# Optimization experiments

Measured on AMD Instinct MI355X. Metric: run time of the kernel, lower is better.

The kernel has to match this reference:

```python
import jax, jax.numpy as jnp
import numpy as np

B = 64           # graph pairs
NPG = 48         # nodes per half-graph
N = B * 2 * NPG  # 6144 nodes
E = B * NPG * NPG  # 147456 directed mapping edges
DEG = 16
EG = N * DEG     # 98304 intra-graph edges
H = 128          # hidden dim (all layers)
HT = H // 2      # time embedding dim
L = 3            # num layers
G = 2 * B        # GraphNorm segments (bn_batch)


def _lin(k, i, o):
    return jax.random.normal(k, (i, o), jnp.float32) * (1.0 / np.sqrt(i))


def setup_inputs():
    key = jax.random.key(0)
    ks = list(jax.random.split(key, 64))
    rng = np.random.default_rng(0)
    inp = {}
    inp["graph_x"] = jax.random.normal(ks[0], (N, H), jnp.float32)
    inp["t"] = jnp.asarray(rng.integers(0, 1000, size=(B,)), jnp.float32)
    inp["noise_mapping_attr"] = jax.random.uniform(ks[1], (E,), jnp.float32)
    # intra-graph edges: random degree-DEG within each half-graph
    halves = np.arange(2 * B)
    bases = (halves // 2) * (2 * NPG) + (halves % 2) * NPG
    base_rep = np.repeat(bases, NPG * DEG)
    gsrc = base_rep + rng.integers(0, NPG, EG)
    gdst = base_rep + rng.integers(0, NPG, EG)
    inp["graph_edge_index"] = jnp.asarray(np.stack([gsrc, gdst]), jnp.int32)
    # full bipartite mapping edges graph1 -> graph2 within each pair
    p = np.repeat(np.arange(B), NPG * NPG)
    i = np.tile(np.repeat(np.arange(NPG), NPG), B)
    j = np.tile(np.tile(np.arange(NPG), NPG), B)
    inp["edge_mapping_idx"] = jnp.asarray(np.stack([p * 2 * NPG + i, p * 2 * NPG + NPG + j]), jnp.int32)
    inp["batch"] = jnp.asarray(np.repeat(np.arange(B), 2 * NPG), jnp.int32)
    inp["x_indicator"] = jnp.asarray(np.tile(np.r_[np.zeros(NPG, np.int32), np.ones(NPG, np.int32)], B), jnp.int32)
    # -------- learned parameters --------
    kit = iter(ks[2:])
    inp["gin_eps"] = jnp.zeros((L,), jnp.float32)
    inp["gin_w1"] = jnp.stack([_lin(next(kit), H, H) for _ in range(L)])
    inp["gin_b1"] = jnp.zeros((L, H), jnp.float32)
    inp["gin_w2"] = jnp.stack([_lin(next(kit), H, H) for _ in range(L)])
    inp["gin_b2"] = jnp.zeros((L, H), jnp.float32)
    inp["gn_w"] = jnp.ones((L, H), jnp.float32)
    inp["gn_b"] = jnp.zeros((L, H), jnp.float32)
    inp["gn_ms"] = jnp.ones((L, H), jnp.float32)
    for nm in ["ag_U", "ag_V", "ag_A", "ag_B", "ag_C"]:
        inp[nm] = jnp.stack([_lin(next(kit), H, H) for _ in range(L)])
        inp[nm + "b"] = jnp.zeros((L, H), jnp.float32)
    inp["ag_T"] = jnp.stack([_lin(next(kit), HT, H) for _ in range(L)])
    inp["ag_Tb"] = jnp.zeros((L, H), jnp.float32)
    inp["tw1"] = _lin(next(kit), H, HT); inp["tb1"] = jnp.zeros((HT,), jnp.float32)
    inp["tw2"] = _lin(next(kit), HT, HT); inp["tb2"] = jnp.zeros((HT,), jnp.float32)
    inp["ew"] = _lin(next(kit), H, H); inp["eb"] = jnp.zeros((H,), jnp.float32)
    inp["mw1"] = _lin(next(kit), H, 2 * H); inp["mb1"] = jnp.zeros((2 * H,), jnp.float32)
    inp["mw2"] = _lin(next(kit), 2 * H, H); inp["mb2"] = jnp.zeros((H,), jnp.float32)
    inp["mw3"] = _lin(next(kit), H, 1); inp["mb3"] = jnp.zeros((1,), jnp.float32)
    return inp


def _forward(graph_x, t, noise_mapping_attr, gin_eps, gin_w1, gin_b1, gin_w2, gin_b2,
             gn_w, gn_b, gn_ms, ag_U, ag_Ub, ag_V, ag_Vb, ag_A, ag_Ab, ag_B, ag_Bb,
             ag_C, ag_Cb, ag_T, ag_Tb, tw1, tb1, tw2, tb2, ew, eb,
             mw1, mb1, mw2, mb2, mw3, mb3,
             graph_edge_index, edge_mapping_idx, batch, x_indicator):
    seg = jax.ops.segment_sum
    # to_undirected on mapping edges: concat with flipped copy (graph1->graph2 only, so no dups)
    und = jnp.concatenate([edge_mapping_idx, edge_mapping_idx[::-1]], axis=1)   # [2, 2E]
    attr = jnp.concatenate([noise_mapping_attr, noise_mapping_attr])            # [2E]
    esrc, edst = und[0], und[1]
    gsrc, gdst = graph_edge_index[0], graph_edge_index[1]
    # diffusion timestep embedding -> time MLP (hidden -> H/2 -> H/2)
    half = H // 2
    freqs = jnp.exp(-jnp.log(10000.0) * jnp.arange(half, dtype=jnp.float32) / half)
    ang = t[:, None] * freqs
    temb = jnp.concatenate([jnp.cos(ang), jnp.sin(ang)], axis=-1)               # [B, H]
    temb = jnp.maximum(temb @ tw1 + tb1, 0.0) @ tw2 + tb2                       # [B, HT]
    # ScalarEmbeddingSine(normalize=False) on edge attrs, then edge_embed linear
    idx = jnp.arange(H)
    dim_t = 10000.0 ** (2.0 * (idx // 2).astype(jnp.float32) / H)
    pos = attr[:, None] / dim_t
    pe = jnp.stack([jnp.sin(pos[:, 0::2]), jnp.cos(pos[:, 1::2])], axis=2).reshape(-1, H)
    e = pe @ ew + eb                                                            # [2E, H]
    bn_batch = batch * 2 + x_indicator                                          # per half-graph segment ids
    e_batch = batch[esrc]                                                       # graph id per mapping edge
    h = graph_x
    for l in range(L):
        # GINConv (train_eps): nn((1+eps)*x + sum_{j->i} x_j)
        z = (1.0 + gin_eps[l]) * h + seg(h[gsrc], gdst, num_segments=N)
        z = jnp.maximum(z @ gin_w1[l] + gin_b1[l], 0.0) @ gin_w2[l] + gin_b2[l]
        # GraphNorm per half-graph, then ReLU
        cnt = seg(jnp.ones((N, 1), z.dtype), bn_batch, num_segments=G)
        mean = seg(z, bn_batch, num_segments=G) / cnt
        zc = z - mean[bn_batch] * gn_ms[l]
        var = seg(zc * zc, bn_batch, num_segments=G) / cnt
        h = jnp.maximum(gn_w[l] * zc / jnp.sqrt(var[bn_batch] + 1e-5) + gn_b[l], 0.0)
        # AGNN: anisotropic gated message passing over mapping edges, time-conditioned
        t_edge = temb[e_batch] @ ag_T[l] + ag_Tb[l]                              # [2E, H]
        e_new = (e @ ag_A[l] + ag_Ab[l]
                 + (h @ ag_B[l] + ag_Bb[l])[esrc]
                 + (h @ ag_C[l] + ag_Cb[l])[edst]
                 + t_edge)
        gate = jax.nn.sigmoid(e_new)
        magg = seg(gate * (h @ ag_V[l] + ag_Vb[l])[esrc], edst, num_segments=N)
        h = h + jnp.maximum(h @ ag_U[l] + ag_Ub[l] + magg, 0.0)
        e = e + jnp.maximum(e_new, 0.0)
    # readout MLP on edge features
    m = jnp.maximum(e @ mw1 + mb1, 0.0)
    m = jnp.maximum(m @ mw2 + mb2, 0.0)
    m = m @ mw3 + mb3                                                            # [2E, 1]
    half_e = m.shape[0] // 2
    # to_undirected coalesce(add) symmetrizes scores; keep edges with graph-1 source
    return m[:half_e] + m[half_e:]                                               # [E, 1]


def reference(graph_x, t, noise_mapping_attr, gin_eps, gin_w1, gin_b1, gin_w2, gin_b2,
              gn_w, gn_b, gn_ms, ag_U, ag_Ub, ag_V, ag_Vb, ag_A, ag_Ab, ag_B, ag_Bb,
              ag_C, ag_Cb, ag_T, ag_Tb, tw1, tb1, tw2, tb2, ew, eb,
              mw1, mb1, mw2, mb2, mw3, mb3,
              graph_edge_index, edge_mapping_idx, batch, x_indicator):
    return _forward(graph_x, t, noise_mapping_attr, gin_eps, gin_w1, gin_b1, gin_w2, gin_b2,
                    gn_w, gn_b, gn_ms, ag_U, ag_Ub, ag_V, ag_Vb, ag_A, ag_Ab, ag_B, ag_Bb,
                    ag_C, ag_Cb, ag_T, ag_Tb, tw1, tb1, tw2, tb2, ew, eb,
                    mw1, mb1, mw2, mb2, mw3, mb3,
                    graph_edge_index, edge_mapping_idx, batch, x_indicator)
```

## Files before the change

kernel.cpp:

```cpp
#include <hip/hip_runtime.h>
#include <cstdint>
#include <cstddef>

constexpr int kB   = 64;
constexpr int kNPG = 48;
constexpr int kN   = 6144;
constexpr int kE   = 147456;
constexpr int kE2  = 294912;
constexpr int kEG  = 98304;
constexpr int kH   = 128;
constexpr int kHT  = 64;
constexpr int kL   = 3;

using short8 = __attribute__((ext_vector_type(8))) short;
using f32x4  = __attribute__((ext_vector_type(4))) float;

__device__ __forceinline__ unsigned short f2bf(float x) {
    unsigned int u = __float_as_uint(x);
    u = (u + 0x7FFFu + ((u >> 16) & 1u)) >> 16;
    return (unsigned short)u;
}
__device__ __forceinline__ float bf2f(unsigned short v) {
    return __uint_as_float(((unsigned int)v) << 16);
}
__device__ __forceinline__ f32x4 mfma16(short8 a, short8 b, f32x4 c) {
    return __builtin_amdgcn_mfma_f32_16x16x32_bf16(a, b, c, 0, 0, 0);
}

__global__ void k_wprep(const float* __restrict__ W, unsigned short* __restrict__ Wf, int N) {
    int lane = threadIdx.x;
    int NT = N >> 4;
    int kt = blockIdx.x / NT, nt = blockIdx.x % NT;
    int k0 = kt * 32 + (lane >> 4) * 8;
    int col = nt * 16 + (lane & 15);
    unsigned short tmp[8];
    #pragma unroll
    for (int j = 0; j < 8; ++j) tmp[j] = f2bf(W[(size_t)(k0 + j) * N + col]);
    unsigned short* dst = Wf + (((size_t)blockIdx.x) * 64 + lane) * 8;
    *(uint4*)dst = *(const uint4*)tmp;
}

__global__ __launch_bounds__(256) void k_pegemm(const float* __restrict__ attr,
                                                const unsigned short* __restrict__ wf,
                                                const float* __restrict__ eb,
                                                uint32_t* __restrict__ e_packed) {
    int t = threadIdx.x, lane = t & 63, w = t >> 6;
    int rowbase = blockIdx.x * 64 + w * 16;
    int arow = rowbase + (lane & 15);
    float av = attr[arow < kE ? arow : arow - kE];
    f32x4 acc[8];
    #pragma unroll
    for (int nt = 0; nt < 8; ++nt) acc[nt] = (f32x4){0.f, 0.f, 0.f, 0.f};
    #pragma unroll
    for (int kt = 0; kt < 4; ++kt) {
        short8 ahi, alo;
        int k0 = kt * 32 + (lane >> 4) * 8;
        #pragma unroll
        for (int j = 0; j < 8; ++j) {
            int k = k0 + j;
            float freq = exp2f(-(float)(k >> 1) * 0.20762050593046264f);
            float ang = av * freq;
            float v = (k & 1) ? __cosf(ang) : __sinf(ang);
            unsigned short h = f2bf(v);
            unsigned short l2 = f2bf(v - bf2f(h));
            ahi[j] = (short)h; alo[j] = (short)l2;
        }
        #pragma unroll
        for (int nt = 0; nt < 8; ++nt) {
            short8 wb = *(const short8*)&wf[(((size_t)kt * 8 + nt) * 64 + lane) * 8];
            acc[nt] = mfma16(ahi, wb, acc[nt]);
            acc[nt] = mfma16(alo, wb, acc[nt]);
        }
    }
    #pragma unroll
    for (int nt = 0; nt < 8; ++nt) {
        int col = nt * 16 + (lane & 15);
        float bb = eb[col];
        #pragma unroll
        for (int reg = 0; reg < 4; ++reg) {
            int row = rowbase + (lane >> 4) * 4 + reg;
            float v = acc[nt][reg] + bb;
            unsigned short h = f2bf(v);
            unsigned short l2 = f2bf(v - bf2f(h));
            e_packed[(size_t)row * kH + col] = (uint32_t)h | ((uint32_t)l2 << 16);
        }
    }
}

__global__ __launch_bounds__(256) void k_egemm(uint32_t* __restrict__ e_packed,
                                               const unsigned short* __restrict__ wfA,
                                               const float* __restrict__ Ab,
                                               const float* __restrict__ tGl,
                                               const float* __restrict__ hB,
                                               const float* __restrict__ hC,
                                               unsigned short* __restrict__ gate) {
    __shared__ float X[48][128];
    __shared__ float Y[4][128];
    __shared__ float Z[128];
    int t = threadIdx.x, lane = t & 63, w = t >> 6;
    int row0 = blockIdx.x * 128;
    int half = row0 >= kE;
    int off = row0 - (half ? kE : 0);
    int p = off / 2304;
    int off2 = off - p * 2304;
    int a0 = off2 / 48, boff = off2 - a0 * 48;
    const float* Xsrc = half ? hB : hC;
    const float* Ysrc = half ? hC : hB;

    if (t < 128) Z[t] = tGl[p * kH + t] + Ab[t];
    for (int i = t; i < 48 * 32; i += 256) {
        int r = i >> 5, c = (i & 31) << 2;
        *(float4*)&X[r][c] = *(const float4*)&Xsrc[(size_t)(p * 96 + 48 + r) * kH + c];
    }
    for (int i = t; i < 4 * 32; i += 256) {
        int r = i >> 5, c = (i & 31) << 2;
        int a = a0 + r; if (a > 47) a = 47;
        *(float4*)&Y[r][c] = *(const float4*)&Ysrc[(size_t)(p * 96 + a) * kH + c];
    }
    __syncthreads();

    f32x4 acc[2][8];
    #pragma unroll
    for (int rt = 0; rt < 2; ++rt)
        #pragma unroll
        for (int nt = 0; nt < 8; ++nt) acc[rt][nt] = (f32x4){0.f, 0.f, 0.f, 0.f};

    #pragma unroll
    for (int kt = 0; kt < 4; ++kt) {
        short8 ahi[2], alo[2];
        #pragma unroll
        for (int rt = 0; rt < 2; ++rt) {
            int row = row0 + w * 32 + rt * 16 + (lane & 15);
            const uint32_t* ep = e_packed + (size_t)row * kH + kt * 32 + (lane >> 4) * 8;
            uint4 q0 = *(const uint4*)ep;
            uint4 q1 = *(const uint4*)(ep + 4);
            uint32_t qs[8] = {q0.x, q0.y, q0.z, q0.w, q1.x, q1.y, q1.z, q1.w};
            #pragma unroll
            for (int j = 0; j < 8; ++j) {
                ahi[rt][j] = (short)(qs[j] & 0xffff);
                alo[rt][j] = (short)(qs[j] >> 16);
            }
        }
        #pragma unroll
        for (int nt = 0; nt < 8; ++nt) {
            short8 wb = *(const short8*)&wfA[(((size_t)kt * 8 + nt) * 64 + lane) * 8];
            #pragma unroll
            for (int rt = 0; rt < 2; ++rt) {
                acc[rt][nt] = mfma16(ahi[rt], wb, acc[rt][nt]);
                acc[rt][nt] = mfma16(alo[rt], wb, acc[rt][nt]);
            }
        }
    }

    #pragma unroll
    for (int rt = 0; rt < 2; ++rt) {
        #pragma unroll
        for (int nt = 0; nt < 8; ++nt) {
            int col = nt * 16 + (lane & 15);
            float zc = Z[col];
            #pragma unroll
            for (int reg = 0; reg < 4; ++reg) {
                int rl = w * 32 + rt * 16 + (lane >> 4) * 4 + reg;
                int idx2 = boff + rl;
                int arel = (idx2 >= 144) ? 3 : (idx2 >= 96) ? 2 : (idx2 >= 48) ? 1 : 0;
                int b = idx2 - arel * 48;
                float v = acc[rt][nt][reg] + zc + Y[arel][col] + X[b][col];
                int grow = row0 + rl;
                float g = 1.f / (1.f + __expf(-v));
                gate[(size_t)grow * kH + col] = f2bf(g);
                uint32_t old = e_packed[(size_t)grow * kH + col];
                float oldv = bf2f((unsigned short)(old & 0xffff)) + bf2f((unsigned short)(old >> 16));
                float ne = oldv + fmaxf(v, 0.f);
                unsigned short h = f2bf(ne);
                unsigned short l2 = f2bf(ne - bf2f(h));
                e_packed[(size_t)grow * kH + col] = (uint32_t)h | ((uint32_t)l2 << 16);
            }
        }
    }
}

__global__ __launch_bounds__(256) void k_readout(const uint32_t* __restrict__ e_packed,
                                                 const unsigned short* __restrict__ wf1,
                                                 const float* __restrict__ mb1,
                                                 const unsigned short* __restrict__ wf2,
                                                 const float* __restrict__ mb2,
                                                 const float* __restrict__ mw3,
                                                 const float* __restrict__ mb3,
                                                 float* __restrict__ partial) {
    __shared__ char smem[64 * 528];
    uint32_t (*eS)[132] = (uint32_t(*)[132])smem;
    unsigned short (*m1S)[264] = (unsigned short(*)[264])smem;
    int t = threadIdx.x, lane = t & 63, w = t >> 6;
    int row0 = blockIdx.x * 64;

    for (int i = t; i < 64 * 32; i += 256) {
        int r = i >> 5, c = (i & 31) << 2;
        *(uint4*)&eS[r][c] = *(const uint4*)&e_packed[(size_t)(row0 + r) * kH + c];
    }
    __syncthreads();

    f32x4 acc1[4][4];
    #pragma unroll
    for (int rt = 0; rt < 4; ++rt)
        #pragma unroll
        for (int n = 0; n < 4; ++n) acc1[rt][n] = (f32x4){0.f, 0.f, 0.f, 0.f};
    #pragma unroll
    for (int kt = 0; kt < 4; ++kt) {
        short8 ahi[4], alo[4];
        #pragma unroll
        for (int rt = 0; rt < 4; ++rt) {
            int r = rt * 16 + (lane & 15);
            const uint32_t* ep = &eS[r][kt * 32 + (lane >> 4) * 8];
            #pragma unroll
            for (int j = 0; j < 8; ++j) {
                uint32_t q = ep[j];
                ahi[rt][j] = (short)(q & 0xffff);
                alo[rt][j] = (short)(q >> 16);
            }
        }
        #pragma unroll
        for (int n = 0; n < 4; ++n) {
            int nt = w * 4 + n;
            short8 wb = *(const short8*)&wf1[(((size_t)kt * 16 + nt) * 64 + lane) * 8];
            #pragma unroll
            for (int rt = 0; rt < 4; ++rt) {
                acc1[rt][n] = mfma16(ahi[rt], wb, acc1[rt][n]);
                acc1[rt][n] = mfma16(alo[rt], wb, acc1[rt][n]);
            }
        }
    }
    __syncthreads();
    #pragma unroll
    for (int rt = 0; rt < 4; ++rt) {
        #pragma unroll
        for (int n = 0; n < 4; ++n) {
            int col = (w * 4 + n) * 16 + (lane & 15);
            float bb = mb1[col];
            #pragma unroll
            for (int reg = 0; reg < 4; ++reg) {
                int r = rt * 16 + (lane >> 4) * 4 + reg;
                m1S[r][col] = f2bf(fmaxf(acc1[rt][n][reg] + bb, 0.f));
            }
        }
    }
    __syncthreads();

    f32x4 acc2[8];
    #pragma unroll
    for (int nt = 0; nt < 8; ++nt) acc2[nt] = (f32x4){0.f, 0.f, 0.f, 0.f};
    #pragma unroll
    for (int kt = 0; kt < 8; ++kt) {
        int r = w * 16 + (lane & 15);
        short8 a2 = *(const short8*)&m1S[r][kt * 32 + (lane >> 4) * 8];
        #pragma unroll
        for (int nt = 0; nt < 8; ++nt) {
            short8 wb = *(const short8*)&wf2[(((size_t)kt * 8 + nt) * 64 + lane) * 8];
            acc2[nt] = mfma16(a2, wb, acc2[nt]);
        }
    }
    float s[4] = {0.f, 0.f, 0.f, 0.f};
    #pragma unroll
    for (int nt = 0; nt < 8; ++nt) {
        int col = nt * 16 + (lane & 15);
        float w3 = mw3[col], bb = mb2[col];
        #pragma unroll
        for (int reg = 0; reg < 4; ++reg)
            s[reg] += fmaxf(acc2[nt][reg] + bb, 0.f) * w3;
    }
    #pragma unroll
    for (int mask = 1; mask <= 8; mask <<= 1)
        #pragma unroll
        for (int reg = 0; reg < 4; ++reg) s[reg] += __shfl_xor(s[reg], mask);
    if ((lane & 15) == 0) {
        float b3 = mb3[0];
        #pragma unroll
        for (int reg = 0; reg < 4; ++reg)
            partial[row0 + w * 16 + (lane >> 4) * 4 + reg] = s[reg] + b3;
    }
}

struct GemmPtrs { const float* W; const float* bias; float* C; };
struct GemmJobs { GemmPtrs j[4]; };

template<int MODE>
__global__ __launch_bounds__(256)
void k_gemm(const float* A, GemmJobs jobs, int M, int K, int Ncol)
{
    const GemmPtrs P = jobs.j[blockIdx.z];
    __shared__ float As[64][36];
    __shared__ float Ws[32][132];
    const int tid = threadIdx.x;
    const int tx = tid & 15, ty = tid >> 4;
    const int row0 = blockIdx.x * 64;
    const int colofs = blockIdx.y * 128;

    float acc[4][8];
    #pragma unroll
    for (int i = 0; i < 4; ++i)
        #pragma unroll
        for (int j = 0; j < 8; ++j) acc[i][j] = 0.f;

    for (int kk = 0; kk < K; kk += 32) {
        #pragma unroll
        for (int it = 0; it < 2; ++it) {
            int q = tid + it * 256;
            int r = q >> 3, kq = (q & 7) << 2;
            *(float4*)&As[r][kq] = *(const float4*)&A[(size_t)(row0 + r) * K + kk + kq];
        }
        #pragma unroll
        for (int it = 0; it < 4; ++it) {
            int q = tid + it * 256;
            int r = q >> 5, c = (q & 31) << 2;
            *(float4*)&Ws[r][c] = *(const float4*)&P.W[(size_t)(kk + r) * Ncol + colofs + c];
        }
        __syncthreads();
        #pragma unroll
        for (int k4 = 0; k4 < 8; ++k4) {
            float4 a[4];
            #pragma unroll
            for (int i = 0; i < 4; ++i)
                a[i] = *(const float4*)&As[ty * 4 + i][k4 * 4];
            float4 wv[4][2];
            #pragma unroll
            for (int k = 0; k < 4; ++k) {
                wv[k][0] = *(const float4*)&Ws[k4 * 4 + k][tx * 4];
                wv[k][1] = *(const float4*)&Ws[k4 * 4 + k][64 + tx * 4];
            }
            #pragma unroll
            for (int i = 0; i < 4; ++i) {
                #pragma unroll
                for (int k = 0; k < 4; ++k) {
                    float av = ((const float*)&a[i])[k];
                    acc[i][0] = fmaf(av, wv[k][0].x, acc[i][0]);
                    acc[i][1] = fmaf(av, wv[k][0].y, acc[i][1]);
                    acc[i][2] = fmaf(av, wv[k][0].z, acc[i][2]);
                    acc[i][3] = fmaf(av, wv[k][0].w, acc[i][3]);
                    acc[i][4] = fmaf(av, wv[k][1].x, acc[i][4]);
                    acc[i][5] = fmaf(av, wv[k][1].y, acc[i][5]);
                    acc[i][6] = fmaf(av, wv[k][1].z, acc[i][6]);
                    acc[i][7] = fmaf(av, wv[k][1].w, acc[i][7]);
                }
            }
        }
        __syncthreads();
    }

    #pragma unroll
    for (int i = 0; i < 4; ++i) {
        int row = row0 + ty * 4 + i;
        #pragma unroll
        for (int g = 0; g < 2; ++g) {
            int c = colofs + g * 64 + tx * 4;
            float4 vo;
            #pragma unroll
            for (int q = 0; q < 4; ++q) {
                float v = acc[i][g * 4 + q] + P.bias[c + q];
                if (MODE == 1) v = fmaxf(v, 0.f);
                ((float*)&vo)[q] = v;
            }
            *(float4*)&P.C[(size_t)row * Ncol + c] = vo;
        }
    }
}

__global__ void k_hist(const int* __restrict__ gdst, int* __restrict__ cnt) {
    int i = blockIdx.x * 256 + threadIdx.x;
    atomicAdd(&cnt[gdst[i]], 1);
}
__global__ void k_scan(const int* __restrict__ cnt, int* __restrict__ rs) {
    __shared__ int part[256];
    int t = threadIdx.x;
    const int per = kN / 256;
    int s = 0;
    for (int i = 0; i < per; ++i) s += cnt[t * per + i];
    part[t] = s;
    __syncthreads();
    if (t == 0) {
        int run = 0;
        for (int i = 0; i < 256; ++i) { int v = part[i]; part[i] = run; run += v; }
        rs[kN] = run;
    }
    __syncthreads();
    int run = part[t];
    for (int i = 0; i < per; ++i) { int idx = t * per + i; rs[idx] = run; run += cnt[idx]; }
}
__global__ void k_scatter(const int* __restrict__ gsrc, const int* __restrict__ gdst,
                          const int* __restrict__ rs, int* __restrict__ cur, int* __restrict__ csr) {
    int i = blockIdx.x * 256 + threadIdx.x;
    int d = gdst[i];
    int pos = atomicAdd(&cur[d], 1);
    csr[rs[d] + pos] = gsrc[i];
}
__global__ void k_gin(const float* __restrict__ h, const int* __restrict__ rs,
                      const int* __restrict__ csr, const float* __restrict__ gin_eps,
                      int l, float* __restrict__ z) {
    int n = blockIdx.x, c = threadIdx.x;
    int s0 = rs[n], s1 = rs[n + 1];
    float acc = 0.f;
    for (int k = s0; k < s1; ++k) acc += h[(size_t)csr[k] * kH + c];
    float eps = gin_eps[l];
    z[(size_t)n * kH + c] = (1.f + eps) * h[(size_t)n * kH + c] + acc;
}
__global__ void k_gnorm(const float* __restrict__ z, const float* __restrict__ gnw,
                        const float* __restrict__ gnb, const float* __restrict__ gnms,
                        float* __restrict__ h) {
    int g = blockIdx.x, c = threadIdx.x;
    size_t base = (size_t)g * 48 * kH + c;
    float sum = 0.f;
    for (int r = 0; r < 48; ++r) sum += z[base + (size_t)r * kH];
    float mean = sum * (1.f / 48.f);
    float mm = mean * gnms[c];
    float var = 0.f;
    for (int r = 0; r < 48; ++r) { float d = z[base + (size_t)r * kH] - mm; var = fmaf(d, d, var); }
    var *= (1.f / 48.f);
    float inv = rsqrtf(var + 1e-5f);
    float w = gnw[c], bb = gnb[c];
    for (int r = 0; r < 48; ++r) {
        float d = z[base + (size_t)r * kH] - mm;
        h[base + (size_t)r * kH] = fmaxf(fmaf(w * d, inv, bb), 0.f);
    }
}
__global__ void k_agg(const unsigned short* __restrict__ gate, const float* __restrict__ hV,
                      const float* __restrict__ hU, float* __restrict__ h) {
    int n = blockIdx.x, c = threadIdx.x;
    int p = n / 96, r = n - (n / 96) * 96;
    float acc = 0.f;
    if (r >= 48) {
        int b = r - 48;
        size_t ebase = (size_t)p * 2304 + b;
        for (int a = 0; a < 48; ++a) {
            size_t eidx = ebase + (size_t)a * 48;
            int src = p * 96 + a;
            acc = fmaf(bf2f(gate[eidx * kH + c]), hV[(size_t)src * kH + c], acc);
        }
    } else {
        int a = r;
        size_t ebase = (size_t)kE + (size_t)p * 2304 + (size_t)a * 48;
        for (int b = 0; b < 48; ++b) {
            int src = p * 96 + 48 + b;
            acc = fmaf(bf2f(gate[(ebase + b) * kH + c]), hV[(size_t)src * kH + c], acc);
        }
    }
    float v = hU[(size_t)n * kH + c] + acc;
    h[(size_t)n * kH + c] += fmaxf(v, 0.f);
}
__global__ void k_temb(const float* __restrict__ t, const float* __restrict__ tw1,
                       const float* __restrict__ tb1, const float* __restrict__ tw2,
                       const float* __restrict__ tb2, float* __restrict__ temb) {
    __shared__ float t0[128];
    __shared__ float h1[64];
    int b = blockIdx.x, j = threadIdx.x;
    float tv = t[b];
    float f = expf(-0.14391156831212787f * (float)j);
    float ang = tv * f;
    t0[j] = cosf(ang);
    t0[j + 64] = sinf(ang);
    __syncthreads();
    float s = tb1[j];
    for (int i = 0; i < 128; ++i) s = fmaf(t0[i], tw1[i * 64 + j], s);
    h1[j] = fmaxf(s, 0.f);
    __syncthreads();
    float s2 = tb2[j];
    for (int i = 0; i < 64; ++i) s2 = fmaf(h1[i], tw2[i * 64 + j], s2);
    temb[b * 64 + j] = s2;
}
__global__ void k_tg(const float* __restrict__ temb, const float* __restrict__ agT,
                     const float* __restrict__ agTb, float* __restrict__ tG) {
    __shared__ float tm[64];
    int bid = blockIdx.x;
    int l = bid >> 6, p = bid & 63, c = threadIdx.x;
    if (c < 64) tm[c] = temb[p * 64 + c];
    __syncthreads();
    const float* T = agT + (size_t)l * 64 * kH;
    float s = agTb[l * kH + c];
    for (int i = 0; i < 64; ++i) s = fmaf(tm[i], T[i * kH + c], s);
    tG[((size_t)l * 64 + p) * kH + c] = s;
}
__global__ void k_final(const float* __restrict__ partial, float* __restrict__ out) {
    int i = blockIdx.x * 256 + threadIdx.x;
    out[i] = partial[i] + partial[i + kE];
}

extern "C" void kernel_launch(void* const* d_in, const int* in_sizes, int n_in,
                              void* d_out, int out_size, void* d_ws, size_t ws_size,
                              hipStream_t stream)
{
    (void)in_sizes; (void)n_in; (void)out_size; (void)ws_size;
    const float* graph_x = (const float*)d_in[0];
    const float* t_in    = (const float*)d_in[1];
    const float* attr    = (const float*)d_in[2];
    const int*   gedge   = (const int*)d_in[3];
    const float* gin_eps = (const float*)d_in[7];
    const float* gin_w1  = (const float*)d_in[8];
    const float* gin_b1  = (const float*)d_in[9];
    const float* gin_w2  = (const float*)d_in[10];
    const float* gin_b2  = (const float*)d_in[11];
    const float* gn_w    = (const float*)d_in[12];
    const float* gn_b    = (const float*)d_in[13];
    const float* gn_ms   = (const float*)d_in[14];
    const float* ag_U    = (const float*)d_in[15];
    const float* ag_Ub   = (const float*)d_in[16];
    const float* ag_V    = (const float*)d_in[17];
    const float* ag_Vb   = (const float*)d_in[18];
    const float* ag_A    = (const float*)d_in[19];
    const float* ag_Ab   = (const float*)d_in[20];
    const float* ag_B    = (const float*)d_in[21];
    const float* ag_Bb   = (const float*)d_in[22];
    const float* ag_C    = (const float*)d_in[23];
    const float* ag_Cb   = (const float*)d_in[24];
    const float* ag_T    = (const float*)d_in[25];
    const float* ag_Tb   = (const float*)d_in[26];
    const float* tw1     = (const float*)d_in[27];
    const float* tb1     = (const float*)d_in[28];
    const float* tw2     = (const float*)d_in[29];
    const float* tb2     = (const float*)d_in[30];
    const float* ew      = (const float*)d_in[31];
    const float* eb      = (const float*)d_in[32];
    const float* mw1     = (const float*)d_in[33];
    const float* mb1     = (const float*)d_in[34];
    const float* mw2     = (const float*)d_in[35];
    const float* mb2     = (const float*)d_in[36];
    const float* mw3     = (const float*)d_in[37];
    const float* mb3     = (const float*)d_in[38];
    float* out = (float*)d_out;

    char* wsb = (char*)d_ws;
    size_t o = 0;
    auto carve = [&](size_t bytes) { char* p = wsb + o; o += (bytes + 255) & ~(size_t)255; return p; };
    uint32_t* e_packed    = (uint32_t*)carve((size_t)kE2 * kH * 4);
    unsigned short* gate  = (unsigned short*)carve((size_t)kE2 * kH * 2);
    float* h              = (float*)carve((size_t)kN * kH * 4);
    float* zb             = (float*)carve((size_t)kN * kH * 4);
    float* z1b            = (float*)carve((size_t)kN * kH * 4);
    float* hB             = (float*)carve((size_t)kN * kH * 4);
    float* hC             = (float*)carve((size_t)kN * kH * 4);
    float* hV             = (float*)carve((size_t)kN * kH * 4);
    float* hU             = (float*)carve((size_t)kN * kH * 4);
    float* temb           = (float*)carve((size_t)kB * kHT * 4);
    float* tG             = (float*)carve((size_t)kL * kB * kH * 4);
    float* partial        = (float*)carve((size_t)kE2 * 4);
    int* cnt              = (int*)carve((size_t)kN * 4);
    int* cur              = (int*)carve((size_t)kN * 4);
    int* rs               = (int*)carve((size_t)(kN + 1) * 4);
    int* csr              = (int*)carve((size_t)kEG * 4);
    unsigned short* wf_ew = (unsigned short*)carve((size_t)kH * kH * 2);
    unsigned short* wf_A  = (unsigned short*)carve((size_t)kL * kH * kH * 2);
    unsigned short* wf_m1 = (unsigned short*)carve((size_t)kH * 256 * 2);
    unsigned short* wf_m2 = (unsigned short*)carve((size_t)256 * kH * 2);

    const int* gsrc = gedge;
    const int* gdst = gedge + kEG;

    hipMemsetAsync(cnt, 0, (size_t)kN * 4, stream);
    hipMemsetAsync(cur, 0, (size_t)kN * 4, stream);
    hipMemcpyAsync(h, graph_x, (size_t)kN * kH * 4, hipMemcpyDeviceToDevice, stream);

    k_hist<<<kEG / 256, 256, 0, stream>>>(gdst, cnt);
    k_scan<<<1, 256, 0, stream>>>(cnt, rs);
    k_scatter<<<kEG / 256, 256, 0, stream>>>(gsrc, gdst, rs, cur, csr);
    k_temb<<<kB, 64, 0, stream>>>(t_in, tw1, tb1, tw2, tb2, temb);
    k_tg<<<kL * kB, kH, 0, stream>>>(temb, ag_T, ag_Tb, tG);

    k_wprep<<<4 * 8, 64, 0, stream>>>(ew, wf_ew, kH);
    for (int l = 0; l < kL; ++l)
        k_wprep<<<4 * 8, 64, 0, stream>>>(ag_A + (size_t)l * kH * kH, wf_A + (size_t)l * kH * kH, kH);
    k_wprep<<<4 * 16, 64, 0, stream>>>(mw1, wf_m1, 256);
    k_wprep<<<8 * 8, 64, 0, stream>>>(mw2, wf_m2, kH);

    k_pegemm<<<kE2 / 64, 256, 0, stream>>>(attr, wf_ew, eb, e_packed);

    for (int l = 0; l < kL; ++l) {
        k_gin<<<kN, kH, 0, stream>>>(h, rs, csr, gin_eps, l, zb);
        {
            GemmJobs jobs = {};
            jobs.j[0] = { gin_w1 + (size_t)l * kH * kH, gin_b1 + (size_t)l * kH, z1b };
            k_gemm<1><<<dim3(kN / 64, 1, 1), 256, 0, stream>>>(zb, jobs, kN, kH, kH);
        }
        {
            GemmJobs jobs = {};
            jobs.j[0] = { gin_w2 + (size_t)l * kH * kH, gin_b2 + (size_t)l * kH, zb };
            k_gemm<0><<<dim3(kN / 64, 1, 1), 256, 0, stream>>>(z1b, jobs, kN, kH, kH);
        }
        k_gnorm<<<128, kH, 0, stream>>>(zb, gn_w + (size_t)l * kH, gn_b + (size_t)l * kH,
                                        gn_ms + (size_t)l * kH, h);
        {
            GemmJobs jobs = {};
            jobs.j[0] = { ag_B + (size_t)l * kH * kH, ag_Bb + (size_t)l * kH, hB };
            jobs.j[1] = { ag_C + (size_t)l * kH * kH, ag_Cb + (size_t)l * kH, hC };
            jobs.j[2] = { ag_V + (size_t)l * kH * kH, ag_Vb + (size_t)l * kH, hV };
            jobs.j[3] = { ag_U + (size_t)l * kH * kH, ag_Ub + (size_t)l * kH, hU };
            k_gemm<0><<<dim3(kN / 64, 1, 4), 256, 0, stream>>>(h, jobs, kN, kH, kH);
        }
        k_egemm<<<kE2 / 128, 256, 0, stream>>>(e_packed, wf_A + (size_t)l * kH * kH,
                                               ag_Ab + (size_t)l * kH, tG + (size_t)l * kB * kH,
                                               hB, hC, gate);
        k_agg<<<kN, kH, 0, stream>>>(gate, hV, hU, h);
    }

    k_readout<<<kE2 / 64, 256, 0, stream>>>(e_packed, wf_m1, mb1, wf_m2, mb2, mw3, mb3, partial);
    k_final<<<kE / 256, 256, 0, stream>>>(partial, out);
}
```

Before: 941.0 us.

## Fuse per-graph node pipeline into one MFMA kernel and skip unused final aggregation

The per-layer node path (GIN neighbour sum, two GIN linear layers, GraphNorm, and the four B/C/V/U projections) is merged into a single kernel with one block per 48-node half-graph. Intermediates stay in shared memory, and the fp32 FMA GEMMs become split-bf16 MFMA GEMMs. All 22 square weight matrices are converted in one batched prep launch. In the last layer the gate store and the node aggregation are skipped, because only edge features feed the readout. The fused kernel launches only 128 blocks and each uses just three of its four waves for the MFMA stages, which trades parallelism for fewer launches and less global traffic.

```diff
diff --git a/kernel.cpp b/kernel.cpp
--- a/kernel.cpp
+++ b/kernel.cpp
@@ -23,8 +23,20 @@
 __device__ __forceinline__ float bf2f(unsigned short v) {
     return __uint_as_float(((unsigned int)v) << 16);
 }
+__device__ __forceinline__ uint32_t packsplit(float v) {
+    unsigned short h = f2bf(v);
+    unsigned short l = f2bf(v - bf2f(h));
+    return (uint32_t)h | ((uint32_t)l << 16);
+}
 __device__ __forceinline__ f32x4 mfma16(short8 a, short8 b, f32x4 c) {
     return __builtin_amdgcn_mfma_f32_16x16x32_bf16(a, b, c, 0, 0, 0);
+}
+__device__ __forceinline__ void loadfrag(const uint32_t* p, short8& hi, short8& lo) {
+    uint4 q0 = *(const uint4*)p;
+    uint4 q1 = *(const uint4*)(p + 4);
+    uint32_t qs[8] = {q0.x, q0.y, q0.z, q0.w, q1.x, q1.y, q1.z, q1.w};
+    #pragma unroll
+    for (int j = 0; j < 8; ++j) { hi[j] = (short)(qs[j] & 0xffff); lo[j] = (short)(qs[j] >> 16); }
 }
 
 __global__ void k_wprep(const float* __restrict__ W, unsigned short* __restrict__ Wf, int N) {
@@ -37,6 +49,21 @@
     #pragma unroll
     for (int j = 0; j < 8; ++j) tmp[j] = f2bf(W[(size_t)(k0 + j) * N + col]);
     unsigned short* dst = Wf + (((size_t)blockIdx.x) * 64 + lane) * 8;
+    *(uint4*)dst = *(const uint4*)tmp;
+}
+
+struct WSrcs { const float* p[22]; };
+__global__ void k_wprep_multi(WSrcs s, unsigned short* __restrict__ Wf) {
+    int lane = threadIdx.x;
+    int mat = blockIdx.x >> 5, tile = blockIdx.x & 31;
+    int kt = tile >> 3, nt = tile & 7;
+    const float* W = s.p[mat];
+    int k0 = kt * 32 + (lane >> 4) * 8;
+    int col = nt * 16 + (lane & 15);
+    unsigned short tmp[8];
+    #pragma unroll
+    for (int j = 0; j < 8; ++j) tmp[j] = f2bf(W[(size_t)(k0 + j) * kH + col]);
+    unsigned short* dst = Wf + (size_t)mat * 16384 + (((size_t)tile) * 64 + lane) * 8;
     *(uint4*)dst = *(const uint4*)tmp;
 }
 
@@ -79,14 +106,190 @@
         #pragma unroll
         for (int reg = 0; reg < 4; ++reg) {
             int row = rowbase + (lane >> 4) * 4 + reg;
-            float v = acc[nt][reg] + bb;
-            unsigned short h = f2bf(v);
-            unsigned short l2 = f2bf(v - bf2f(h));
-            e_packed[(size_t)row * kH + col] = (uint32_t)h | ((uint32_t)l2 << 16);
-        }
-    }
-}
-
+            e_packed[(size_t)row * kH + col] = packsplit(acc[nt][reg] + bb);
+        }
+    }
+}
+
+__global__ __launch_bounds__(256) void k_node(
+    float* __restrict__ h,
+    int l, const int* __restrict__ rs, const int* __restrict__ csr,
+    const float* __restrict__ gin_eps,
+    const unsigned short* __restrict__ wf_g1, const float* __restrict__ b1,
+    const unsigned short* __restrict__ wf_g2, const float* __restrict__ b2,
+    const float* __restrict__ gnw, const float* __restrict__ gnb, const float* __restrict__ gnms,
+    const unsigned short* __restrict__ wf_B, const float* __restrict__ Bb,
+    const unsigned short* __restrict__ wf_C, const float* __restrict__ Cb,
+    const unsigned short* __restrict__ wf_V, const float* __restrict__ Vb,
+    const unsigned short* __restrict__ wf_U, const float* __restrict__ Ub,
+    float* __restrict__ hB, float* __restrict__ hC, float* __restrict__ hV, float* __restrict__ hU)
+{
+    __shared__ char sA[48 * 132 * 4];
+    __shared__ char sB[48 * 132 * 4];
+    __shared__ float mmS[128], aS[128], red0[128], red1[128];
+    float    (*hS)[132]   = (float(*)[132])sA;
+    uint32_t (*m1pk)[132] = (uint32_t(*)[132])sA;
+    uint32_t (*hnpk)[132] = (uint32_t(*)[132])sA;
+    uint32_t (*zpk)[132]  = (uint32_t(*)[132])sB;
+    float    (*z2S)[132]  = (float(*)[132])sB;
+    int t = threadIdx.x, lane = t & 63, w = t >> 6;
+    int g = blockIdx.x, nbase = g * 48;
+
+    for (int i = t; i < 48 * 128; i += 256) {
+        int r = i >> 7, c = i & 127;
+        hS[r][c] = h[(size_t)(nbase + r) * kH + c];
+    }
+    __syncthreads();
+
+    {
+        float eps1 = 1.f + gin_eps[l];
+        int c = t & 127;
+        for (int rp = t >> 7; rp < 48; rp += 2) {
+            float acc = eps1 * hS[rp][c];
+            int s0 = rs[nbase + rp], s1 = rs[nbase + rp + 1];
+            for (int k = s0; k < s1; ++k) {
+                int s = csr[k] - nbase;
+                acc += hS[s][c];
+            }
+            zpk[rp][c] = packsplit(acc);
+        }
+    }
+    __syncthreads();
+
+    {
+        f32x4 acc1[8];
+        if (w < 3) {
+            #pragma unroll
+            for (int nt = 0; nt < 8; ++nt) acc1[nt] = (f32x4){0.f, 0.f, 0.f, 0.f};
+            #pragma unroll
+            for (int kt = 0; kt < 4; ++kt) {
+                short8 hi, lo;
+                loadfrag(&zpk[w * 16 + (lane & 15)][kt * 32 + (lane >> 4) * 8], hi, lo);
+                #pragma unroll
+                for (int nt = 0; nt < 8; ++nt) {
+                    short8 wb = *(const short8*)&wf_g1[(((size_t)kt * 8 + nt) * 64 + lane) * 8];
+                    acc1[nt] = mfma16(hi, wb, acc1[nt]);
+                    acc1[nt] = mfma16(lo, wb, acc1[nt]);
+                }
+            }
+        }
+        __syncthreads();
+        if (w < 3) {
+            #pragma unroll
+            for (int nt = 0; nt < 8; ++nt) {
+                int col = nt * 16 + (lane & 15);
+                float bb = b1[col];
+                #pragma unroll
+                for (int reg = 0; reg < 4; ++reg) {
+                    int row = w * 16 + (lane >> 4) * 4 + reg;
+                    m1pk[row][col] = packsplit(fmaxf(acc1[nt][reg] + bb, 0.f));
+                }
+            }
+        }
+    }
+    __syncthreads();
+
+    {
+        f32x4 acc2[8];
+        if (w < 3) {
+            #pragma unroll
+            for (int nt = 0; nt < 8; ++nt) acc2[nt] = (f32x4){0.f, 0.f, 0.f, 0.f};
+            #pragma unroll
+            for (int kt = 0; kt < 4; ++kt) {
+                short8 hi, lo;
+                loadfrag(&m1pk[w * 16 + (lane & 15)][kt * 32 + (lane >> 4) * 8], hi, lo);
+                #pragma unroll
+                for (int nt = 0; nt < 8; ++nt) {
+                    short8 wb = *(const short8*)&wf_g2[(((size_t)kt * 8 + nt) * 64 + lane) * 8];
+                    acc2[nt] = mfma16(hi, wb, acc2[nt]);
+                    acc2[nt] = mfma16(lo, wb, acc2[nt]);
+                }
+            }
+        }
+        __syncthreads();
+        if (w < 3) {
+            #pragma unroll
+            for (int nt = 0; nt < 8; ++nt) {
+                int col = nt * 16 + (lane & 15);
+                float bb = b2[col];
+                #pragma unroll
+                for (int reg = 0; reg < 4; ++reg) {
+                    int row = w * 16 + (lane >> 4) * 4 + reg;
+                    z2S[row][col] = acc2[nt][reg] + bb;
+                }
+            }
+        }
+    }
+    __syncthreads();
+
+    {
+        int c = t & 127, hh = t >> 7;
+        float s = 0.f;
+        for (int r = hh * 24; r < hh * 24 + 24; ++r) s += z2S[r][c];
+        if (hh == 0) red0[c] = s; else red1[c] = s;
+        __syncthreads();
+        if (t < 128) {
+            float mean = (red0[t] + red1[t]) * (1.f / 48.f);
+            mmS[t] = mean * gnms[t];
+        }
+        __syncthreads();
+        float mm = mmS[c];
+        float s2 = 0.f;
+        for (int r = hh * 24; r < hh * 24 + 24; ++r) { float d = z2S[r][c] - mm; s2 = fmaf(d, d, s2); }
+        if (hh == 0) red0[c] = s2; else red1[c] = s2;
+        __syncthreads();
+        if (t < 128) {
+            float var = (red0[t] + red1[t]) * (1.f / 48.f);
+            aS[t] = gnw[t] * rsqrtf(var + 1e-5f);
+        }
+    }
+    __syncthreads();
+
+    for (int i = t; i < 48 * 128; i += 256) {
+        int r = i >> 7, c = i & 127;
+        float hn = fmaxf(aS[c] * (z2S[r][c] - mmS[c]) + gnb[c], 0.f);
+        h[(size_t)(nbase + r) * kH + c] = hn;
+        hnpk[r][c] = packsplit(hn);
+    }
+    __syncthreads();
+
+    {
+        const unsigned short* wfs[4] = {wf_B, wf_C, wf_V, wf_U};
+        const float* bs[4] = {Bb, Cb, Vb, Ub};
+        float* outs[4] = {hB, hC, hV, hU};
+        #pragma unroll 4
+        for (int m = 0; m < 4; ++m) {
+            if (w < 3) {
+                f32x4 accp[8];
+                #pragma unroll
+                for (int nt = 0; nt < 8; ++nt) accp[nt] = (f32x4){0.f, 0.f, 0.f, 0.f};
+                #pragma unroll
+                for (int kt = 0; kt < 4; ++kt) {
+                    short8 hi, lo;
+                    loadfrag(&hnpk[w * 16 + (lane & 15)][kt * 32 + (lane >> 4) * 8], hi, lo);
+                    #pragma unroll
+                    for (int nt = 0; nt < 8; ++nt) {
+                        short8 wb = *(const short8*)&wfs[m][(((size_t)kt * 8 + nt) * 64 + lane) * 8];
+                        accp[nt] = mfma16(hi, wb, accp[nt]);
+                        accp[nt] = mfma16(lo, wb, accp[nt]);
+                    }
+                }
+                #pragma unroll
+                for (int nt = 0; nt < 8; ++nt) {
+                    int col = nt * 16 + (lane & 15);
+                    float bb = bs[m][col];
+                    #pragma unroll
+                    for (int reg = 0; reg < 4; ++reg) {
+                        int row = w * 16 + (lane >> 4) * 4 + reg;
+                        outs[m][(size_t)(nbase + row) * kH + col] = accp[nt][reg] + bb;
+                    }
+                }
+            }
+        }
+    }
+}
+
+template<bool GATE>
 __global__ __launch_bounds__(256) void k_egemm(uint32_t* __restrict__ e_packed,
                                                const unsigned short* __restrict__ wfA,
                                                const float* __restrict__ Ab,
@@ -127,27 +330,19 @@
 
     #pragma unroll
     for (int kt = 0; kt < 4; ++kt) {
-        short8 ahi[2], alo[2];
+        short8 hi[2], lo[2];
         #pragma unroll
         for (int rt = 0; rt < 2; ++rt) {
             int row = row0 + w * 32 + rt * 16 + (lane & 15);
-            const uint32_t* ep = e_packed + (size_t)row * kH + kt * 32 + (lane >> 4) * 8;
-            uint4 q0 = *(const uint4*)ep;
-            uint4 q1 = *(const uint4*)(ep + 4);
-            uint32_t qs[8] = {q0.x, q0.y, q0.z, q0.w, q1.x, q1.y, q1.z, q1.w};
-            #pragma unroll
-            for (int j = 0; j < 8; ++j) {
-                ahi[rt][j] = (short)(qs[j] & 0xffff);
-                alo[rt][j] = (short)(qs[j] >> 16);
-            }
+            loadfrag(e_packed + (size_t)row * kH + kt * 32 + (lane >> 4) * 8, hi[rt], lo[rt]);
         }
         #pragma unroll
         for (int nt = 0; nt < 8; ++nt) {
             short8 wb = *(const short8*)&wfA[(((size_t)kt * 8 + nt) * 64 + lane) * 8];
             #pragma unroll
             for (int rt = 0; rt < 2; ++rt) {
-                acc[rt][nt] = mfma16(ahi[rt], wb, acc[rt][nt]);
-                acc[rt][nt] = mfma16(alo[rt], wb, acc[rt][nt]);
+                acc[rt][nt] = mfma16(hi[rt], wb, acc[rt][nt]);
+                acc[rt][nt] = mfma16(lo[rt], wb, acc[rt][nt]);
             }
         }
     }
@@ -166,17 +361,42 @@
                 int b = idx2 - arel * 48;
                 float v = acc[rt][nt][reg] + zc + Y[arel][col] + X[b][col];
                 int grow = row0 + rl;
-                float g = 1.f / (1.f + __expf(-v));
-                gate[(size_t)grow * kH + col] = f2bf(g);
+                if (GATE) {
+                    float g = 1.f / (1.f + __expf(-v));
+                    gate[(size_t)grow * kH + col] = f2bf(g);
+                }
                 uint32_t old = e_packed[(size_t)grow * kH + col];
-                float oldv = bf2f((unsigned short)(old & 0xffff)) + bf2f((unsigned short)(old >> 16));
-                float ne = oldv + fmaxf(v, 0.f);
-                unsigned short h = f2bf(ne);
-                unsigned short l2 = f2bf(ne - bf2f(h));
-                e_packed[(size_t)grow * kH + col] = (uint32_t)h | ((uint32_t)l2 << 16);
-            }
-        }
-    }
+                float ne = bf2f((unsigned short)(old & 0xffff)) + bf2f((unsigned short)(old >> 16))
+                           + fmaxf(v, 0.f);
+                e_packed[(size_t)grow * kH + col] = packsplit(ne);
+            }
+        }
+    }
+}
+
+__global__ void k_agg(const unsigned short* __restrict__ gate, const float* __restrict__ hV,
+                      const float* __restrict__ hU, float* __restrict__ h) {
+    int n = blockIdx.x, c = threadIdx.x;
+    int p = n / 96, r = n - (n / 96) * 96;
+    float acc = 0.f;
+    if (r >= 48) {
+        int b = r - 48;
+        size_t ebase = (size_t)p * 2304 + b;
+        for (int a = 0; a < 48; ++a) {
+            size_t eidx = ebase + (size_t)a * 48;
+            int src = p * 96 + a;
+            acc = fmaf(bf2f(gate[eidx * kH + c]), hV[(size_t)src * kH + c], acc);
+        }
+    } else {
+        int a = r;
+        size_t ebase = (size_t)kE + (size_t)p * 2304 + (size_t)a * 48;
+        for (int b = 0; b < 48; ++b) {
+            int src = p * 96 + 48 + b;
+            acc = fmaf(bf2f(gate[(ebase + b) * kH + c]), hV[(size_t)src * kH + c], acc);
+        }
+    }
+    float v = hU[(size_t)n * kH + c] + acc;
+    h[(size_t)n * kH + c] += fmaxf(v, 0.f);
 }
 
 __global__ __launch_bounds__(256) void k_readout(const uint32_t* __restrict__ e_packed,
@@ -208,16 +428,8 @@
     for (int kt = 0; kt < 4; ++kt) {
         short8 ahi[4], alo[4];
         #pragma unroll
-        for (int rt = 0; rt < 4; ++rt) {
-            int r = rt * 16 + (lane & 15);
-            const uint32_t* ep = &eS[r][kt * 32 + (lane >> 4) * 8];
-            #pragma unroll
-            for (int j = 0; j < 8; ++j) {
-                uint32_t q = ep[j];
-                ahi[rt][j] = (short)(q & 0xffff);
-                alo[rt][j] = (short)(q >> 16);
-            }
-        }
+        for (int rt = 0; rt < 4; ++rt)
+            loadfrag(&eS[rt * 16 + (lane & 15)][kt * 32 + (lane >> 4) * 8], ahi[rt], alo[rt]);
         #pragma unroll
         for (int n = 0; n < 4; ++n) {
             int nt = w * 4 + n;
@@ -276,90 +488,6 @@
         #pragma unroll
         for (int reg = 0; reg < 4; ++reg)
             partial[row0 + w * 16 + (lane >> 4) * 4 + reg] = s[reg] + b3;
-    }
-}
-
-struct GemmPtrs { const float* W; const float* bias; float* C; };
-struct GemmJobs { GemmPtrs j[4]; };
-
-template<int MODE>
-__global__ __launch_bounds__(256)
-void k_gemm(const float* A, GemmJobs jobs, int M, int K, int Ncol)
-{
-    const GemmPtrs P = jobs.j[blockIdx.z];
-    __shared__ float As[64][36];
-    __shared__ float Ws[32][132];
-    const int tid = threadIdx.x;
-    const int tx = tid & 15, ty = tid >> 4;
-    const int row0 = blockIdx.x * 64;
-    const int colofs = blockIdx.y * 128;
-
-    float acc[4][8];
-    #pragma unroll
-    for (int i = 0; i < 4; ++i)
-        #pragma unroll
-        for (int j = 0; j < 8; ++j) acc[i][j] = 0.f;
-
-    for (int kk = 0; kk < K; kk += 32) {
-        #pragma unroll
-        for (int it = 0; it < 2; ++it) {
-            int q = tid + it * 256;
-            int r = q >> 3, kq = (q & 7) << 2;
-            *(float4*)&As[r][kq] = *(const float4*)&A[(size_t)(row0 + r) * K + kk + kq];
-        }
-        #pragma unroll
-        for (int it = 0; it < 4; ++it) {
-            int q = tid + it * 256;
-            int r = q >> 5, c = (q & 31) << 2;
-            *(float4*)&Ws[r][c] = *(const float4*)&P.W[(size_t)(kk + r) * Ncol + colofs + c];
-        }
-        __syncthreads();
-        #pragma unroll
-        for (int k4 = 0; k4 < 8; ++k4) {
-            float4 a[4];
-            #pragma unroll
-            for (int i = 0; i < 4; ++i)
-                a[i] = *(const float4*)&As[ty * 4 + i][k4 * 4];
-            float4 wv[4][2];
-            #pragma unroll
-            for (int k = 0; k < 4; ++k) {
-                wv[k][0] = *(const float4*)&Ws[k4 * 4 + k][tx * 4];
-                wv[k][1] = *(const float4*)&Ws[k4 * 4 + k][64 + tx * 4];
-            }
-            #pragma unroll
-            for (int i = 0; i < 4; ++i) {
-                #pragma unroll
-                for (int k = 0; k < 4; ++k) {
-                    float av = ((const float*)&a[i])[k];
-                    acc[i][0] = fmaf(av, wv[k][0].x, acc[i][0]);
-                    acc[i][1] = fmaf(av, wv[k][0].y, acc[i][1]);
-                    acc[i][2] = fmaf(av, wv[k][0].z, acc[i][2]);
-                    acc[i][3] = fmaf(av, wv[k][0].w, acc[i][3]);
-                    acc[i][4] = fmaf(av, wv[k][1].x, acc[i][4]);
-                    acc[i][5] = fmaf(av, wv[k][1].y, acc[i][5]);
-                    acc[i][6] = fmaf(av, wv[k][1].z, acc[i][6]);
-                    acc[i][7] = fmaf(av, wv[k][1].w, acc[i][7]);
-                }
-            }
-        }
-        __syncthreads();
-    }
-
-    #pragma unroll
-    for (int i = 0; i < 4; ++i) {
-        int row = row0 + ty * 4 + i;
-        #pragma unroll
-        for (int g = 0; g < 2; ++g) {
-            int c = colofs + g * 64 + tx * 4;
-            float4 vo;
-            #pragma unroll
-            for (int q = 0; q < 4; ++q) {
-                float v = acc[i][g * 4 + q] + P.bias[c + q];
-                if (MODE == 1) v = fmaxf(v, 0.f);
-                ((float*)&vo)[q] = v;
-            }
-            *(float4*)&P.C[(size_t)row * Ncol + c] = vo;
-        }
     }
 }
 
@@ -390,59 +518,6 @@
     int d = gdst[i];
     int pos = atomicAdd(&cur[d], 1);
     csr[rs[d] + pos] = gsrc[i];
-}
-__global__ void k_gin(const float* __restrict__ h, const int* __restrict__ rs,
-                      const int* __restrict__ csr, const float* __restrict__ gin_eps,
-                      int l, float* __restrict__ z) {
-    int n = blockIdx.x, c = threadIdx.x;
-    int s0 = rs[n], s1 = rs[n + 1];
-    float acc = 0.f;
-    for (int k = s0; k < s1; ++k) acc += h[(size_t)csr[k] * kH + c];
-    float eps = gin_eps[l];
-    z[(size_t)n * kH + c] = (1.f + eps) * h[(size_t)n * kH + c] + acc;
-}
-__global__ void k_gnorm(const float* __restrict__ z, const float* __restrict__ gnw,
-                        const float* __restrict__ gnb, const float* __restrict__ gnms,
-                        float* __restrict__ h) {
-    int g = blockIdx.x, c = threadIdx.x;
-    size_t base = (size_t)g * 48 * kH + c;
-    float sum = 0.f;
-    for (int r = 0; r < 48; ++r) sum += z[base + (size_t)r * kH];
-    float mean = sum * (1.f / 48.f);
-    float mm = mean * gnms[c];
-    float var = 0.f;
-    for (int r = 0; r < 48; ++r) { float d = z[base + (size_t)r * kH] - mm; var = fmaf(d, d, var); }
-    var *= (1.f / 48.f);
-    float inv = rsqrtf(var + 1e-5f);
-    float w = gnw[c], bb = gnb[c];
-    for (int r = 0; r < 48; ++r) {
-        float d = z[base + (size_t)r * kH] - mm;
-        h[base + (size_t)r * kH] = fmaxf(fmaf(w * d, inv, bb), 0.f);
-    }
-}
-__global__ void k_agg(const unsigned short* __restrict__ gate, const float* __restrict__ hV,
-                      const float* __restrict__ hU, float* __restrict__ h) {
-    int n = blockIdx.x, c = threadIdx.x;
-    int p = n / 96, r = n - (n / 96) * 96;
-    float acc = 0.f;
-    if (r >= 48) {
-        int b = r - 48;
-        size_t ebase = (size_t)p * 2304 + b;
-        for (int a = 0; a < 48; ++a) {
-            size_t eidx = ebase + (size_t)a * 48;
-            int src = p * 96 + a;
-            acc = fmaf(bf2f(gate[eidx * kH + c]), hV[(size_t)src * kH + c], acc);
-        }
-    } else {
-        int a = r;
-        size_t ebase = (size_t)kE + (size_t)p * 2304 + (size_t)a * 48;
-        for (int b = 0; b < 48; ++b) {
-            int src = p * 96 + 48 + b;
-            acc = fmaf(bf2f(gate[(ebase + b) * kH + c]), hV[(size_t)src * kH + c], acc);
-        }
-    }
-    float v = hU[(size_t)n * kH + c] + acc;
-    h[(size_t)n * kH + c] += fmaxf(v, 0.f);
 }
 __global__ void k_temb(const float* __restrict__ t, const float* __restrict__ tw1,
                        const float* __restrict__ tb1, const float* __restrict__ tw2,
@@ -530,8 +605,6 @@
     uint32_t* e_packed    = (uint32_t*)carve((size_t)kE2 * kH * 4);
     unsigned short* gate  = (unsigned short*)carve((size_t)kE2 * kH * 2);
     float* h              = (float*)carve((size_t)kN * kH * 4);
-    float* zb             = (float*)carve((size_t)kN * kH * 4);
-    float* z1b            = (float*)carve((size_t)kN * kH * 4);
     float* hB             = (float*)carve((size_t)kN * kH * 4);
     float* hC             = (float*)carve((size_t)kN * kH * 4);
     float* hV             = (float*)carve((size_t)kN * kH * 4);
@@ -543,8 +616,7 @@
     int* cur              = (int*)carve((size_t)kN * 4);
     int* rs               = (int*)carve((size_t)(kN + 1) * 4);
     int* csr              = (int*)carve((size_t)kEG * 4);
-    unsigned short* wf_ew = (unsigned short*)carve((size_t)kH * kH * 2);
-    unsigned short* wf_A  = (unsigned short*)carve((size_t)kL * kH * kH * 2);
+    unsigned short* wf_all = (unsigned short*)carve((size_t)22 * 16384 * 2);
     unsigned short* wf_m1 = (unsigned short*)carve((size_t)kH * 256 * 2);
     unsigned short* wf_m2 = (unsigned short*)carve((size_t)256 * kH * 2);
 
@@ -561,40 +633,47 @@
     k_temb<<<kB, 64, 0, stream>>>(t_in, tw1, tb1, tw2, tb2, temb);
     k_tg<<<kL * kB, kH, 0, stream>>>(temb, ag_T, ag_Tb, tG);
 
-    k_wprep<<<4 * 8, 64, 0, stream>>>(ew, wf_ew, kH);
-    for (int l = 0; l < kL; ++l)
-        k_wprep<<<4 * 8, 64, 0, stream>>>(ag_A + (size_t)l * kH * kH, wf_A + (size_t)l * kH * kH, kH);
+    {
+        WSrcs s;
+        s.p[0] = ew;
+        for (int l = 0; l < 3; ++l) {
+            s.p[1 + l]  = ag_A   + (size_t)l * kH * kH;
+            s.p[4 + l]  = gin_w1 + (size_t)l * kH * kH;
+            s.p[7 + l]  = gin_w2 + (size_t)l * kH * kH;
+            s.p[10 + l] = ag_B   + (size_t)l * kH * kH;
+            s.p[13 + l] = ag_C   + (size_t)l * kH * kH;
+            s.p[16 + l] = ag_V   + (size_t)l * kH * kH;
+            s.p[19 + l] = ag_U   + (size_t)l * kH * kH;
+        }
+        k_wprep_multi<<<22 * 32, 64, 0, stream>>>(s, wf_all);
+    }
     k_wprep<<<4 * 16, 64, 0, stream>>>(mw1, wf_m1, 256);
     k_wprep<<<8 * 8, 64, 0, stream>>>(mw2, wf_m2, kH);
 
-    k_pegemm<<<kE2 / 64, 256, 0, stream>>>(attr, wf_ew, eb, e_packed);
-
+    k_pegemm<<<kE2 / 64, 256, 0, stream>>>(attr, wf_all , eb, e_packed);
+
+    auto wf = [&](int idx) { return wf_all + (size_t)idx * 16384; };
     for (int l = 0; l < kL; ++l) {
-        k_gin<<<kN, kH, 0, stream>>>(h, rs, csr, gin_eps, l, zb);
-        {
-            GemmJobs jobs = {};
-            jobs.j[0] = { gin_w1 + (size_t)l * kH * kH, gin_b1 + (size_t)l * kH, z1b };
-            k_gemm<1><<<dim3(kN / 64, 1, 1), 256, 0, stream>>>(zb, jobs, kN, kH, kH);
-        }
-        {
-            GemmJobs jobs = {};
-            jobs.j[0] = { gin_w2 + (size_t)l * kH * kH, gin_b2 + (size_t)l * kH, zb };
-            k_gemm<0><<<dim3(kN / 64, 1, 1), 256, 0, stream>>>(z1b, jobs, kN, kH, kH);
-        }
-        k_gnorm<<<128, kH, 0, stream>>>(zb, gn_w + (size_t)l * kH, gn_b + (size_t)l * kH,
-                                        gn_ms + (size_t)l * kH, h);
-        {
-            GemmJobs jobs = {};
-            jobs.j[0] = { ag_B + (size_t)l * kH * kH, ag_Bb + (size_t)l * kH, hB };
-            jobs.j[1] = { ag_C + (size_t)l * kH * kH, ag_Cb + (size_t)l * kH, hC };
-            jobs.j[2] = { ag_V + (size_t)l * kH * kH, ag_Vb + (size_t)l * kH, hV };
-            jobs.j[3] = { ag_U + (size_t)l * kH * kH, ag_Ub + (size_t)l * kH, hU };
-            k_gemm<0><<<dim3(kN / 64, 1, 4), 256, 0, stream>>>(h, jobs, kN, kH, kH);
-        }
-        k_egemm<<<kE2 / 128, 256, 0, stream>>>(e_packed, wf_A + (size_t)l * kH * kH,
-                                               ag_Ab + (size_t)l * kH, tG + (size_t)l * kB * kH,
-                                               hB, hC, gate);
-        k_agg<<<kN, kH, 0, stream>>>(gate, hV, hU, h);
+        k_node<<<128, 256, 0, stream>>>(
+            h, l, rs, csr, gin_eps,
+            wf(4 + l), gin_b1 + (size_t)l * kH,
+            wf(7 + l), gin_b2 + (size_t)l * kH,
+            gn_w + (size_t)l * kH, gn_b + (size_t)l * kH, gn_ms + (size_t)l * kH,
+            wf(10 + l), ag_Bb + (size_t)l * kH,
+            wf(13 + l), ag_Cb + (size_t)l * kH,
+            wf(16 + l), ag_Vb + (size_t)l * kH,
+            wf(19 + l), ag_Ub + (size_t)l * kH,
+            hB, hC, hV, hU);
+        if (l < kL - 1) {
+            k_egemm<true><<<kE2 / 128, 256, 0, stream>>>(
+                e_packed, wf(1 + l), ag_Ab + (size_t)l * kH, tG + (size_t)l * kB * kH,
+                hB, hC, gate);
+            k_agg<<<kN, kH, 0, stream>>>(gate, hV, hU, h);
+        } else {
+            k_egemm<false><<<kE2 / 128, 256, 0, stream>>>(
+                e_packed, wf(1 + l), ag_Ab + (size_t)l * kH, tG + (size_t)l * kB * kH,
+                hB, hC, gate);
+        }
     }
 
     k_readout<<<kE2 / 64, 256, 0, stream>>>(e_packed, wf_m1, mb1, wf_m2, mb2, mw3, mb3, partial);
```

New measurement: 964.8 us. 1.03x slower.
